# Kernel optimization log

Hardware: AMD Instinct MI355X
Metric: run time of the kernel (lower is better)

The kernel has to match this reference:

```python
import jax, jax.numpy as jnp
import numpy as np

DEG = 3
KNOTS = np.array([i / 9.0 for i in range(1, 9)], dtype=np.float32)  # 8 knots in (0,1)
SDIM = DEG + 1 + len(KNOTS)  # 12
B, D_IN, D_HID, D_OUT = 32768, 256, 256, 1


def spline_basis(t):
    # TruncatedPowerBasis: [1, t, t^2, t^3, relu(t-k)^3 ...]  -> (B, SDIM)
    powers = t[:, None] ** jnp.arange(DEG + 1, dtype=t.dtype)
    knots = jnp.asarray(KNOTS, dtype=t.dtype)
    spl = jax.nn.relu(t[:, None] - knots[None, :]) ** DEG
    return jnp.concatenate([powers, spl], axis=1)


def vc_layer(x, basis, W, b, in_dim, out_dim):
    # Mathematically identical to torch: W_b = basis @ W (viewed (in,out)); out = x @ W_b + basis @ b
    # Factored to avoid materializing the (B, in, out) per-sample weight tensor.
    Ws = W.reshape(SDIM, in_dim, out_dim)
    tmp = jnp.einsum('bi,sio->bso', x, Ws)        # (B, SDIM, out)
    return jnp.einsum('bs,bso->bo', basis, tmp) + basis @ b


def setup_inputs() -> dict:
    key = jax.random.key(0)
    ks = jax.random.split(key, 8)
    xavier = lambda k, shape: jax.random.uniform(
        k, shape, dtype=jnp.float32,
        minval=-1.0, maxval=1.0) * np.sqrt(6.0 / (shape[0] + shape[1]))
    return {
        'treatment': jax.random.uniform(ks[0], (B,), dtype=jnp.float32),
        'features': jax.random.normal(ks[1], (B, D_IN), dtype=jnp.float32),
        'W0': xavier(ks[2], (SDIM, D_IN * D_HID)),
        'b0': xavier(ks[3], (SDIM, D_HID)),
        'W1': xavier(ks[4], (SDIM, D_HID * D_HID)),
        'b1': xavier(ks[5], (SDIM, D_HID)),
        'W2': xavier(ks[6], (SDIM, D_HID * D_OUT)),
        'b2': xavier(ks[7], (SDIM, D_OUT)),
    }


def reference(treatment, features, W0, b0, W1, b1, W2, b2):
    basis = spline_basis(treatment)                     # (B, SDIM)
    x = vc_layer(features, basis, W0, b0, D_IN, D_HID)
    x = jax.nn.relu(x)
    x = vc_layer(x, basis, W1, b1, D_HID, D_HID)
    x = jax.nn.relu(x)
    x = vc_layer(x, basis, W2, b2, D_HID, D_OUT)        # (B, 1)
    return x
```

## Files before the change

kernel.cpp:

```cpp
#include <hip/hip_runtime.h>


typedef __attribute__((ext_vector_type(8))) _Float16 half8;
typedef __attribute__((ext_vector_type(4))) _Float16 half4;
typedef __attribute__((ext_vector_type(4))) float floatx4;

#define XPAD 264

__device__ __forceinline__ void gload16(const _Float16* g, _Float16* l){
  __builtin_amdgcn_global_load_lds(
      (const __attribute__((address_space(1))) void*)g,
      (__attribute__((address_space(3))) void*)l, 16, 0, 0);
}

__device__ __forceinline__ void stage_b(const _Float16* wt, _Float16* slot,
                                        int w, int l){
  gload16(wt +        w * 512 + l * 8, slot +        w * 512);
  gload16(wt + 4096 + w * 512 + l * 8, slot + 4096 + w * 512);
}

__device__ __forceinline__ void make_basis(float t, float* p){
  p[0] = 1.f; p[1] = t; p[2] = t*t; p[3] = p[2]*t;
  const float knots[8] = {1.f/9.f, 2.f/9.f, 3.f/9.f, 4.f/9.f,
                          5.f/9.f, 6.f/9.f, 7.f/9.f, 8.f/9.f};
  #pragma unroll
  for (int j = 0; j < 8; ++j){
    float d = t - knots[j];
    d = fmaxf(d, 0.f);
    p[4+j] = d*d*d;
  }
}

__global__ __launch_bounds__(256)
void pack_w_kernel(const float* __restrict__ W0, const float* __restrict__ W1,
                   _Float16* __restrict__ Wp0, _Float16* __restrict__ Wp1){
  __shared__ float wl[32 * 260];
  const int blk = blockIdx.x;
  const float* W = (blk < 96) ? W0 : W1;
  _Float16* Wp   = (blk < 96) ? Wp0 : Wp1;
  const int c    = (blk < 96) ? blk : blk - 96;
  const int tid  = threadIdx.x;
  const float* src = W + (size_t)c * 8192;
  #pragma unroll
  for (int it = 0; it < 8; ++it){
    int idx = it * 256 + tid;
    int r = idx >> 6, c4 = idx & 63;
    float4 v = *(const float4*)(src + (size_t)idx * 4);
    float* d = &wl[r * 260 + c4 * 4];
    d[0] = v.x; d[1] = v.y; d[2] = v.z; d[3] = v.w;
  }
  __syncthreads();
  const int tpos = (c & 7) * 12 + (c >> 3);
  _Float16* dst = Wp + (size_t)tpos * 8192;
  #pragma unroll
  for (int w = 0; w < 4; ++w){
    int v = w * 256 + tid;
    int n16 = v & 15, qq = (v >> 4) & 3, ntg = v >> 6;
    half8 o;
    #pragma unroll
    for (int j = 0; j < 8; ++j)
      o[j] = (_Float16)wl[(qq * 8 + j) * 260 + ntg * 16 + n16];
    *(half8*)(dst + (size_t)v * 8) = o;
  }
}

__device__ __forceinline__ void gemm_kloop(const _Float16* Xl, _Float16* Bl,
                                           const float* bldsT,
                                           const _Float16* __restrict__ wp,
                                           unsigned xbase, int wm, int wn,
                                           int l16, int w, int l,
                                           floatx4 acc[4][4]){
  const unsigned bbase = (unsigned)(wn * 2048 + l * 8);
  half8 xc[4], xn[4], bc[4], bn[4];
  stage_b(wp + 2 * 8192, Bl + 2 * 8192, w, l);
  #pragma unroll
  for (int nt = 0; nt < 4; ++nt)
    bc[nt] = *(const half8*)(Bl + bbase + nt * 512);
  #pragma unroll
  for (int mt = 0; mt < 4; ++mt)
    xc[mt] = *(const half8*)&Xl[xbase + mt * 16 * XPAD];
  floatx4 btc = *(const floatx4*)&bldsT[wm * 64 + l16 * 4];

  for (int ko = 0; ko < 8; ++ko){
    #pragma unroll
    for (int s = 0; s < 12; ++s){
      __asm__ __volatile__("s_waitcnt vmcnt(2)" ::: "memory");
      __builtin_amdgcn_sched_barrier(0);
      __builtin_amdgcn_s_barrier();
      __builtin_amdgcn_sched_barrier(0);

      #pragma unroll
      for (int nt = 0; nt < 4; ++nt)
        bn[nt] = *(const half8*)(Bl + ((s + 1) & 3) * 8192 + bbase + nt * 512);
      const int sn = (s == 11) ? 0 : s + 1;
      floatx4 btn = *(const floatx4*)&bldsT[sn * 128 + wm * 64 + l16 * 4];
      if (s == 0){
        const int kon = (ko + 1) & 7;
        #pragma unroll
        for (int mt = 0; mt < 4; ++mt)
          xn[mt] = *(const half8*)&Xl[xbase + kon * 32 + mt * 16 * XPAD];
      }

      _Float16 bh[4];
      #pragma unroll
      for (int mt = 0; mt < 4; ++mt) bh[mt] = (_Float16)btc[mt];
      half8 az[4];
      #pragma unroll
      for (int mt = 0; mt < 4; ++mt) az[mt] = xc[mt] * bh[mt];
      #pragma unroll
      for (int mt = 0; mt < 4; ++mt)
        #pragma unroll
        for (int nt = 0; nt < 4; ++nt)
          acc[mt][nt] = __builtin_amdgcn_mfma_f32_16x16x32_f16(
              az[mt], bc[nt], acc[mt][nt], 0, 0, 0);

      #pragma unroll
      for (int nt = 0; nt < 4; ++nt) bc[nt] = bn[nt];
      btc = btn;
      if (s == 11){
        #pragma unroll
        for (int mt = 0; mt < 4; ++mt) xc[mt] = xn[mt];
      }
      stage_b(wp + (size_t)(ko * 12 + s + 3) * 8192,
              Bl + ((s + 3) & 3) * 8192, w, l);
    }
  }
}

__device__ __forceinline__ void add_bias(const float* blds, const float* __restrict__ bias,
                                         int wm, int wn, int q, int l16,
                                         floatx4 acc[4][4]){
  for (int s = 0; s < 12; ++s){
    float bl[4];
    #pragma unroll
    for (int nt = 0; nt < 4; ++nt)
      bl[nt] = bias[s * 256 + wn * 64 + nt * 16 + l16];
    floatx4 bs[4];
    #pragma unroll
    for (int mt = 0; mt < 4; ++mt)
      bs[mt] = *(const floatx4*)&blds[s * 128 + wm * 64 + mt * 16 + q * 4];
    #pragma unroll
    for (int mt = 0; mt < 4; ++mt)
      #pragma unroll
      for (int nt = 0; nt < 4; ++nt)
        #pragma unroll
        for (int r = 0; r < 4; ++r)
          acc[mt][nt][r] += bs[mt][r] * bl[nt];
  }
}

__device__ __forceinline__ void scatter_to_xl(_Float16* Xl, floatx4 acc[4][4],
                                              int wm, int wn, int q, int l16){
  #pragma unroll
  for (int mt = 0; mt < 4; ++mt)
    #pragma unroll
    for (int nt = 0; nt < 4; ++nt)
      #pragma unroll
      for (int r = 0; r < 4; ++r)
        Xl[(wm * 64 + mt * 16 + q * 4 + r) * XPAD + wn * 64 + nt * 16 + l16] =
            (_Float16)fmaxf(acc[mt][nt][r], 0.f);
}

__global__ __launch_bounds__(512, 2)
void fused_all_kernel(const float* __restrict__ feat, const float* __restrict__ treat,
                      const _Float16* __restrict__ Wp0, const float* __restrict__ b0,
                      const _Float16* __restrict__ Wp1, const float* __restrict__ b1,
                      const float* __restrict__ W2, const float* __restrict__ b2,
                      float* __restrict__ out){
  __shared__ _Float16 Xl[128 * XPAD];
  __shared__ _Float16 Bl[4 * 8192];
  __shared__ float blds[12 * 128];
  __shared__ float bldsT[12 * 128];
  __shared__ float w2l[12 * 256];
  __shared__ float redbuf[128 * 4];
  __shared__ float b2l[12];

  const int tid  = threadIdx.x;
  const int m0   = blockIdx.x * 128;
  const int lane = tid & 63;
  const int wid  = tid >> 6;
  const int wm   = wid >> 2;
  const int wn   = wid & 3;
  const int q    = lane >> 4;
  const int l16  = lane & 15;

  stage_b(Wp0,        Bl,        wid, lane);
  stage_b(Wp0 + 8192, Bl + 8192, wid, lane);

  #pragma unroll
  for (int it = 0; it < 16; ++it){
    int idx = it * 512 + tid;
    int m = idx >> 6, c = idx & 63;
    float4 v = *(const float4*)(feat + (size_t)(m0 + m) * 256 + c * 4);
    half4 h = { (_Float16)v.x, (_Float16)v.y, (_Float16)v.z, (_Float16)v.w };
    *(half4*)&Xl[m * XPAD + c * 4] = h;
  }
  #pragma unroll
  for (int it = 0; it < 6; ++it)
    w2l[it * 512 + tid] = W2[it * 512 + tid];
  if (tid < 12) b2l[tid] = b2[tid];
  if (tid < 128){
    float t = treat[m0 + tid];
    float p[12]; make_basis(t, p);
    const int r   = tid;
    const int tmt = (r >> 4) & 3;
    const int tl  = r & 15;
    const int twm = r >> 6;
    #pragma unroll
    for (int s = 0; s < 12; ++s){
      blds [s * 128 + r] = p[s];
      bldsT[s * 128 + twm * 64 + tl * 4 + tmt] = p[s];
    }
  }
  __syncthreads();

  const unsigned xbase = (unsigned)(wm * 64 + l16) * XPAD + q * 8;

  const floatx4 zero = {0.f, 0.f, 0.f, 0.f};
  floatx4 acc[4][4];
  #pragma unroll
  for (int mt = 0; mt < 4; ++mt)
    #pragma unroll
    for (int nt = 0; nt < 4; ++nt) acc[mt][nt] = zero;

  gemm_kloop(Xl, Bl, bldsT, Wp0, xbase, wm, wn, l16, wid, lane, acc);
  add_bias(blds, b0, wm, wn, q, l16, acc);
  __syncthreads();
  scatter_to_xl(Xl, acc, wm, wn, q, l16);
  stage_b(Wp1,        Bl,        wid, lane);
  stage_b(Wp1 + 8192, Bl + 8192, wid, lane);
  __syncthreads();

  #pragma unroll
  for (int mt = 0; mt < 4; ++mt)
    #pragma unroll
    for (int nt = 0; nt < 4; ++nt) acc[mt][nt] = zero;
  gemm_kloop(Xl, Bl, bldsT, Wp1, xbase, wm, wn, l16, wid, lane, acc);
  add_bias(blds, b1, wm, wn, q, l16, acc);

  #pragma unroll
  for (int mt = 0; mt < 4; ++mt)
    #pragma unroll
    for (int nt = 0; nt < 4; ++nt)
      #pragma unroll
      for (int r = 0; r < 4; ++r)
        acc[mt][nt][r] = fmaxf(acc[mt][nt][r], 0.f);
  float outp[4][4];
  #pragma unroll
  for (int mt = 0; mt < 4; ++mt)
    #pragma unroll
    for (int r = 0; r < 4; ++r) outp[mt][r] = 0.f;
  for (int s = 0; s < 12; ++s){
    float w2v[4];
    #pragma unroll
    for (int nt = 0; nt < 4; ++nt)
      w2v[nt] = w2l[s * 256 + wn * 64 + nt * 16 + l16];
    floatx4 bs[4];
    #pragma unroll
    for (int mt = 0; mt < 4; ++mt)
      bs[mt] = *(const floatx4*)&blds[s * 128 + wm * 64 + mt * 16 + q * 4];
    #pragma unroll
    for (int mt = 0; mt < 4; ++mt)
      #pragma unroll
      for (int r = 0; r < 4; ++r){
        float tmp = acc[mt][0][r] * w2v[0] + acc[mt][1][r] * w2v[1]
                  + acc[mt][2][r] * w2v[2] + acc[mt][3][r] * w2v[3];
        outp[mt][r] += bs[mt][r] * tmp;
      }
  }
  #pragma unroll
  for (int mt = 0; mt < 4; ++mt)
    #pragma unroll
    for (int r = 0; r < 4; ++r){
      float v = outp[mt][r];
      v += __shfl_xor(v, 1, 64);
      v += __shfl_xor(v, 2, 64);
      v += __shfl_xor(v, 4, 64);
      v += __shfl_xor(v, 8, 64);
      outp[mt][r] = v;
    }
  if (l16 == 0){
    #pragma unroll
    for (int mt = 0; mt < 4; ++mt)
      #pragma unroll
      for (int r = 0; r < 4; ++r){
        int row = wm * 64 + mt * 16 + q * 4 + r;
        redbuf[row * 4 + wn] = outp[mt][r];
      }
  }
  __syncthreads();
  if (tid < 128){
    float v = redbuf[tid * 4 + 0] + redbuf[tid * 4 + 1]
            + redbuf[tid * 4 + 2] + redbuf[tid * 4 + 3];
    float bb = 0.f;
    #pragma unroll
    for (int s = 0; s < 12; ++s) bb += blds[s * 128 + tid] * b2l[s];
    out[m0 + tid] = v + bb;
  }
}

extern "C" void kernel_launch(void* const* d_in, const int* in_sizes, int n_in,
                              void* d_out, int out_size, void* d_ws, size_t ws_size,
                              hipStream_t stream){
  const float* treat = (const float*)d_in[0];
  const float* feat  = (const float*)d_in[1];
  const float* W0    = (const float*)d_in[2];
  const float* b0    = (const float*)d_in[3];
  const float* W1    = (const float*)d_in[4];
  const float* b1    = (const float*)d_in[5];
  const float* W2    = (const float*)d_in[6];
  const float* b2    = (const float*)d_in[7];

  char* ws = (char*)d_ws;
  _Float16* Wp0 = (_Float16*)(ws);
  _Float16* Wp1 = (_Float16*)(ws + 1572864);
  float* out = (float*)d_out;

  pack_w_kernel<<<192, 256, 0, stream>>>(W0, W1, Wp0, Wp1);
  fused_all_kernel<<<256, 512, 0, stream>>>(feat, treat, Wp0, b0, Wp1, b1,
                                            W2, b2, out);
}
```

Measured before the change: 176.4 us.

## Give each wave a private double-buffered weight slice to drop per-step block barriers

Weight staging moves from a block-shared 4-slot LDS ring to a private 2-slot LDS buffer per wave. Each wave now fetches only the N-quarter of the weight tile it consumes, so the block-wide s_barrier on every k-step can go, leaving only a wave-local vmcnt wait. The B register prefetch and next-X prefetch are also dropped, so operands are read from LDS in the same step. In exchange, the two waves that share an N-quarter each fetch the same weights, which doubles weight traffic from L2. LDS reuse within a wave now relies on wait counts alone, and the prefetch distance shrinks from three steps to two.

```diff
diff --git a/kernel.cpp b/kernel.cpp
--- a/kernel.cpp
+++ b/kernel.cpp
@@ -13,10 +13,12 @@
       (__attribute__((address_space(3))) void*)l, 16, 0, 0);
 }
 
-__device__ __forceinline__ void stage_b(const _Float16* wt, _Float16* slot,
-                                        int w, int l){
-  gload16(wt +        w * 512 + l * 8, slot +        w * 512);
-  gload16(wt + 4096 + w * 512 + l * 8, slot + 4096 + w * 512);
+__device__ __forceinline__ void stage_q(const _Float16* wt, _Float16* slot,
+                                        int wn, int l){
+  const _Float16* src = wt + wn * 2048 + l * 8;
+  #pragma unroll
+  for (int c = 0; c < 4; ++c)
+    gload16(src + c * 512, slot + c * 512);
 }
 
 __device__ __forceinline__ void make_basis(float t, float* p){
@@ -64,46 +66,32 @@
   }
 }
 
-__device__ __forceinline__ void gemm_kloop(const _Float16* Xl, _Float16* Bl,
+__device__ __forceinline__ void gemm_kloop(const _Float16* Xl, _Float16* Bp,
                                            const float* bldsT,
                                            const _Float16* __restrict__ wp,
                                            unsigned xbase, int wm, int wn,
-                                           int l16, int w, int l,
+                                           int l16, int lane,
                                            floatx4 acc[4][4]){
-  const unsigned bbase = (unsigned)(wn * 2048 + l * 8);
-  half8 xc[4], xn[4], bc[4], bn[4];
-  stage_b(wp + 2 * 8192, Bl + 2 * 8192, w, l);
-  #pragma unroll
-  for (int nt = 0; nt < 4; ++nt)
-    bc[nt] = *(const half8*)(Bl + bbase + nt * 512);
-  #pragma unroll
-  for (int mt = 0; mt < 4; ++mt)
-    xc[mt] = *(const half8*)&Xl[xbase + mt * 16 * XPAD];
-  floatx4 btc = *(const floatx4*)&bldsT[wm * 64 + l16 * 4];
-
+  half8 xc[4];
   for (int ko = 0; ko < 8; ++ko){
     #pragma unroll
     for (int s = 0; s < 12; ++s){
-      __asm__ __volatile__("s_waitcnt vmcnt(2)" ::: "memory");
+      __asm__ __volatile__("s_waitcnt vmcnt(4)" ::: "memory");
       __builtin_amdgcn_sched_barrier(0);
-      __builtin_amdgcn_s_barrier();
-      __builtin_amdgcn_sched_barrier(0);
-
-      #pragma unroll
-      for (int nt = 0; nt < 4; ++nt)
-        bn[nt] = *(const half8*)(Bl + ((s + 1) & 3) * 8192 + bbase + nt * 512);
-      const int sn = (s == 11) ? 0 : s + 1;
-      floatx4 btn = *(const floatx4*)&bldsT[sn * 128 + wm * 64 + l16 * 4];
+
       if (s == 0){
-        const int kon = (ko + 1) & 7;
         #pragma unroll
         for (int mt = 0; mt < 4; ++mt)
-          xn[mt] = *(const half8*)&Xl[xbase + kon * 32 + mt * 16 * XPAD];
+          xc[mt] = *(const half8*)&Xl[xbase + ko * 32 + mt * 16 * XPAD];
       }
-
+      half8 bc[4];
+      #pragma unroll
+      for (int nt = 0; nt < 4; ++nt)
+        bc[nt] = *(const half8*)(Bp + (s & 1) * 2048 + nt * 512 + lane * 8);
+      floatx4 bt = *(const floatx4*)&bldsT[s * 128 + wm * 64 + l16 * 4];
       _Float16 bh[4];
       #pragma unroll
-      for (int mt = 0; mt < 4; ++mt) bh[mt] = (_Float16)btc[mt];
+      for (int mt = 0; mt < 4; ++mt) bh[mt] = (_Float16)bt[mt];
       half8 az[4];
       #pragma unroll
       for (int mt = 0; mt < 4; ++mt) az[mt] = xc[mt] * bh[mt];
@@ -114,15 +102,8 @@
           acc[mt][nt] = __builtin_amdgcn_mfma_f32_16x16x32_f16(
               az[mt], bc[nt], acc[mt][nt], 0, 0, 0);
 
-      #pragma unroll
-      for (int nt = 0; nt < 4; ++nt) bc[nt] = bn[nt];
-      btc = btn;
-      if (s == 11){
-        #pragma unroll
-        for (int mt = 0; mt < 4; ++mt) xc[mt] = xn[mt];
-      }
-      stage_b(wp + (size_t)(ko * 12 + s + 3) * 8192,
-              Bl + ((s + 3) & 3) * 8192, w, l);
+      stage_q(wp + (size_t)(ko * 12 + s + 2) * 8192,
+              Bp + (s & 1) * 2048, wn, lane);
     }
   }
 }
@@ -168,7 +149,7 @@
                       const float* __restrict__ W2, const float* __restrict__ b2,
                       float* __restrict__ out){
   __shared__ _Float16 Xl[128 * XPAD];
-  __shared__ _Float16 Bl[4 * 8192];
+  __shared__ _Float16 Bl[8 * 4096];
   __shared__ float blds[12 * 128];
   __shared__ float bldsT[12 * 128];
   __shared__ float w2l[12 * 256];
@@ -183,9 +164,10 @@
   const int wn   = wid & 3;
   const int q    = lane >> 4;
   const int l16  = lane & 15;
-
-  stage_b(Wp0,        Bl,        wid, lane);
-  stage_b(Wp0 + 8192, Bl + 8192, wid, lane);
+  _Float16* Bp   = Bl + wid * 4096;
+
+  stage_q(Wp0,        Bp,        wn, lane);
+  stage_q(Wp0 + 8192, Bp + 2048, wn, lane);
 
   #pragma unroll
   for (int it = 0; it < 16; ++it){
@@ -223,19 +205,19 @@
     #pragma unroll
     for (int nt = 0; nt < 4; ++nt) acc[mt][nt] = zero;
 
-  gemm_kloop(Xl, Bl, bldsT, Wp0, xbase, wm, wn, l16, wid, lane, acc);
+  gemm_kloop(Xl, Bp, bldsT, Wp0, xbase, wm, wn, l16, lane, acc);
   add_bias(blds, b0, wm, wn, q, l16, acc);
   __syncthreads();
   scatter_to_xl(Xl, acc, wm, wn, q, l16);
-  stage_b(Wp1,        Bl,        wid, lane);
-  stage_b(Wp1 + 8192, Bl + 8192, wid, lane);
+  stage_q(Wp1,        Bp,        wn, lane);
+  stage_q(Wp1 + 8192, Bp + 2048, wn, lane);
   __syncthreads();
 
   #pragma unroll
   for (int mt = 0; mt < 4; ++mt)
     #pragma unroll
     for (int nt = 0; nt < 4; ++nt) acc[mt][nt] = zero;
-  gemm_kloop(Xl, Bl, bldsT, Wp1, xbase, wm, wn, l16, wid, lane, acc);
+  gemm_kloop(Xl, Bp, bldsT, Wp1, xbase, wm, wn, l16, lane, acc);
   add_bias(blds, b1, wm, wn, q, l16, acc);
 
   #pragma unroll
```

After: 186.5 us. +5.7%, slower.

## Load packed weights directly from global into registers, dropping LDS staging and barriers

Applied to the files above, without the earlier changes.

Replaces the LDS ring buffer fed by global_load_lds for the B weight tiles with direct per-wave global loads of MFMA fragments, prefetched one step ahead. This removes the per-step waitcnt and workgroup barrier and frees the 64KB Bl buffer. In exchange, waves sharing a B tile each fetch it from global/L2, and load latency is hidden only by a one-step register prefetch. The launch-bounds occupancy hint of two blocks per CU is also dropped.

```diff
diff --git a/kernel.cpp b/kernel.cpp
--- a/kernel.cpp
+++ b/kernel.cpp
@@ -6,18 +6,6 @@
 typedef __attribute__((ext_vector_type(4))) float floatx4;
 
 #define XPAD 264
-
-__device__ __forceinline__ void gload16(const _Float16* g, _Float16* l){
-  __builtin_amdgcn_global_load_lds(
-      (const __attribute__((address_space(1))) void*)g,
-      (__attribute__((address_space(3))) void*)l, 16, 0, 0);
-}
-
-__device__ __forceinline__ void stage_b(const _Float16* wt, _Float16* slot,
-                                        int w, int l){
-  gload16(wt +        w * 512 + l * 8, slot +        w * 512);
-  gload16(wt + 4096 + w * 512 + l * 8, slot + 4096 + w * 512);
-}
 
 __device__ __forceinline__ void make_basis(float t, float* p){
   p[0] = 1.f; p[1] = t; p[2] = t*t; p[3] = p[2]*t;
@@ -64,18 +52,14 @@
   }
 }
 
-__device__ __forceinline__ void gemm_kloop(const _Float16* Xl, _Float16* Bl,
-                                           const float* bldsT,
-                                           const _Float16* __restrict__ wp,
-                                           unsigned xbase, int wm, int wn,
-                                           int l16, int w, int l,
+__device__ __forceinline__ void gemm_kloop(const _Float16* Xl, const float* bldsT,
+                                           const _Float16* __restrict__ wb,
+                                           unsigned xbase, int wm, int l16,
                                            floatx4 acc[4][4]){
-  const unsigned bbase = (unsigned)(wn * 2048 + l * 8);
   half8 xc[4], xn[4], bc[4], bn[4];
-  stage_b(wp + 2 * 8192, Bl + 2 * 8192, w, l);
   #pragma unroll
   for (int nt = 0; nt < 4; ++nt)
-    bc[nt] = *(const half8*)(Bl + bbase + nt * 512);
+    bc[nt] = *(const half8*)(wb + nt * 512);
   #pragma unroll
   for (int mt = 0; mt < 4; ++mt)
     xc[mt] = *(const half8*)&Xl[xbase + mt * 16 * XPAD];
@@ -84,14 +68,10 @@
   for (int ko = 0; ko < 8; ++ko){
     #pragma unroll
     for (int s = 0; s < 12; ++s){
-      __asm__ __volatile__("s_waitcnt vmcnt(2)" ::: "memory");
-      __builtin_amdgcn_sched_barrier(0);
-      __builtin_amdgcn_s_barrier();
-      __builtin_amdgcn_sched_barrier(0);
-
+      const int t = ko * 12 + s;
       #pragma unroll
       for (int nt = 0; nt < 4; ++nt)
-        bn[nt] = *(const half8*)(Bl + ((s + 1) & 3) * 8192 + bbase + nt * 512);
+        bn[nt] = *(const half8*)(wb + (size_t)(t + 1) * 8192 + nt * 512);
       const int sn = (s == 11) ? 0 : s + 1;
       floatx4 btn = *(const floatx4*)&bldsT[sn * 128 + wm * 64 + l16 * 4];
       if (s == 0){
@@ -121,8 +101,6 @@
         #pragma unroll
         for (int mt = 0; mt < 4; ++mt) xc[mt] = xn[mt];
       }
-      stage_b(wp + (size_t)(ko * 12 + s + 3) * 8192,
-              Bl + ((s + 3) & 3) * 8192, w, l);
     }
   }
 }
@@ -161,14 +139,13 @@
             (_Float16)fmaxf(acc[mt][nt][r], 0.f);
 }
 
-__global__ __launch_bounds__(512, 2)
+__global__ __launch_bounds__(512)
 void fused_all_kernel(const float* __restrict__ feat, const float* __restrict__ treat,
                       const _Float16* __restrict__ Wp0, const float* __restrict__ b0,
                       const _Float16* __restrict__ Wp1, const float* __restrict__ b1,
                       const float* __restrict__ W2, const float* __restrict__ b2,
                       float* __restrict__ out){
   __shared__ _Float16 Xl[128 * XPAD];
-  __shared__ _Float16 Bl[4 * 8192];
   __shared__ float blds[12 * 128];
   __shared__ float bldsT[12 * 128];
   __shared__ float w2l[12 * 256];
@@ -183,9 +160,6 @@
   const int wn   = wid & 3;
   const int q    = lane >> 4;
   const int l16  = lane & 15;
-
-  stage_b(Wp0,        Bl,        wid, lane);
-  stage_b(Wp0 + 8192, Bl + 8192, wid, lane);
 
   #pragma unroll
   for (int it = 0; it < 16; ++it){
@@ -215,6 +189,8 @@
   __syncthreads();
 
   const unsigned xbase = (unsigned)(wm * 64 + l16) * XPAD + q * 8;
+  const _Float16* wb0 = Wp0 + wn * 2048 + lane * 8;
+  const _Float16* wb1 = Wp1 + wn * 2048 + lane * 8;
 
   const floatx4 zero = {0.f, 0.f, 0.f, 0.f};
   floatx4 acc[4][4];
@@ -223,19 +199,17 @@
     #pragma unroll
     for (int nt = 0; nt < 4; ++nt) acc[mt][nt] = zero;
 
-  gemm_kloop(Xl, Bl, bldsT, Wp0, xbase, wm, wn, l16, wid, lane, acc);
+  gemm_kloop(Xl, bldsT, wb0, xbase, wm, l16, acc);
   add_bias(blds, b0, wm, wn, q, l16, acc);
   __syncthreads();
   scatter_to_xl(Xl, acc, wm, wn, q, l16);
-  stage_b(Wp1,        Bl,        wid, lane);
-  stage_b(Wp1 + 8192, Bl + 8192, wid, lane);
   __syncthreads();
 
   #pragma unroll
   for (int mt = 0; mt < 4; ++mt)
     #pragma unroll
     for (int nt = 0; nt < 4; ++nt) acc[mt][nt] = zero;
-  gemm_kloop(Xl, Bl, bldsT, Wp1, xbase, wm, wn, l16, wid, lane, acc);
+  gemm_kloop(Xl, bldsT, wb1, xbase, wm, l16, acc);
   add_bias(blds, b1, wm, wn, q, l16, acc);
 
   #pragma unroll
```

Result: slower. 389.0 us (+120.5%).
